# Kernel tuning notes

Measured on AMD Instinct MI355X. Metric: run time of the kernel, lower is better.

The kernel has to match this reference:

```python
import jax, jax.numpy as jnp
import numpy as np

# ---- fixed structural constants from the module source ----
BODY_PARTS = [[1, 2, 3], [4, 5, 6], [0, 7, 8, 9, 10], [11, 12, 13], [14, 15, 16]]
PART_EDGES = [[0, 2], [1, 2], [2, 3], [2, 4]]
N_JOINTS, N_PARTS = 17, 5
K_CHEB = 3  # ChebConv K=2 -> K+1 = 3 polynomial terms


def _pool_scatter_mats():
    # P[p, j] = 1/len(part_p) for j in part_p  (AdaptiveAvgPool1d(1) == mean)
    P = np.zeros((N_PARTS, N_JOINTS), np.float32)
    # S[j, p] = 1 if joint j belongs to part p (broadcast scatter)
    S = np.zeros((N_JOINTS, N_PARTS), np.float32)
    for p, idxs in enumerate(BODY_PARTS):
        for j in idxs:
            P[p, j] = 1.0 / len(idxs)
            S[j, p] = 1.0
    return jnp.asarray(P), jnp.asarray(S)


def _part_adj():
    # adj_mx_from_edges: symmetrize, add self loops, row-normalize
    A = np.zeros((N_PARTS, N_PARTS), np.float32)
    for i, j in PART_EDGES:
        A[i, j] = 1.0
    A = A + A.T  # edges are one-directional and disjoint -> symmetrize
    A = A + np.eye(N_PARTS, dtype=np.float32)
    A = A / A.sum(axis=1, keepdims=True)  # row-normalize
    return jnp.asarray(A)


def _cheb_basis(adj):
    # get_laplacian(normalize=True): L = I - D^{-1/2} A D^{-1/2}
    d_isqrt = jnp.sum(adj, axis=-1) ** (-0.5)
    L = jnp.eye(N_PARTS, dtype=adj.dtype) - (d_isqrt[:, None] * adj) * d_isqrt[None, :]
    I = jnp.eye(N_PARTS, dtype=adj.dtype)
    T2 = 2.0 * (L @ L) - I  # Chebyshev recurrence, K=2
    return jnp.stack([I, L, T2], axis=0)  # [3, 5, 5]


def setup_inputs() -> dict:
    key = jax.random.key(0)
    k1, k2 = jax.random.split(key)
    B, D = 8192, 512
    x = jax.random.normal(k1, (B, N_JOINTS, D), dtype=jnp.float32)
    # xavier-normal-like init for ChebConv weight [K+1, 1, in_c, out_c]
    scale = (2.0 / (D + D)) ** 0.5
    weight = jax.random.normal(k2, (K_CHEB, 1, D, D), dtype=jnp.float32) * scale
    bias = jnp.zeros((1, 1, D), dtype=jnp.float32)
    return {"x": x, "weight": weight, "bias": bias}


def reference(x, weight, bias):
    # x: [B, 17, D]; weight: [3, 1, D, D]; bias: [1, 1, D]
    P, S = _pool_scatter_mats()
    cheb = _cheb_basis(_part_adj())            # [3, 5, 5]
    part_feats = jnp.einsum('pj,bjd->bpd', P, x)              # part-wise mean pool
    prop = jnp.einsum('knm,bmd->kbnd', cheb, part_feats)      # Cheb propagation
    part_out = jnp.einsum('kbnd,kde->bne', prop, weight[:, 0]) + bias[0]  # [B, 5, D]
    return jnp.einsum('jp,bpd->bjd', S, part_out)             # broadcast to 17 joints
```

## Files before the change

kernel.cpp:

```cpp
#include <hip/hip_runtime.h>
#include <hip/hip_bf16.h>
#include <stdint.h>
#include <stddef.h>

typedef __attribute__((ext_vector_type(8))) short short8;
typedef __attribute__((ext_vector_type(4))) float f32x4;
typedef __attribute__((ext_vector_type(4))) unsigned int u32x4;

#define DIM   512
#define NJ    17
#define NPART 5
#define NB    8192
#define KDIM  1536
#define QROWS (NB*NPART)
#define ROWB  (KDIM*2)

struct Cheb { float c[3][5][5]; };

__device__ __forceinline__ void gload_lds16(const void* g, void* l) {
  __builtin_amdgcn_global_load_lds((__attribute__((address_space(1))) void*)(g),
                                   (__attribute__((address_space(3))) void*)(l),
                                   16, 0, 0);
}

__global__ __launch_bounds__(256) void pool_cheb_kernel(
    const float* __restrict__ x, __hip_bfloat16* __restrict__ Q, Cheb cb) {
  int gid = blockIdx.x * 256 + threadIdx.x;
  int b  = gid >> 7;
  int c4 = gid & 127;
  const float* xb = x + (size_t)b * (NJ * DIM) + (c4 << 2);

  f32x4 pf[5];
#pragma unroll
  for (int p = 0; p < 5; ++p) pf[p] = (f32x4){0.f, 0.f, 0.f, 0.f};

  constexpr int jpart[NJ] = {2,0,0,0,1,1,1,2,2,2,2,3,3,3,4,4,4};
#pragma unroll
  for (int j = 0; j < NJ; ++j) {
    f32x4 a = __builtin_nontemporal_load(
        reinterpret_cast<const f32x4*>(xb + j * DIM));
    pf[jpart[j]] += a;
  }
  constexpr float scl[5] = {1.f/3.f, 1.f/3.f, 0.2f, 1.f/3.f, 1.f/3.f};
#pragma unroll
  for (int p = 0; p < 5; ++p) pf[p] *= scl[p];

  char* qb = reinterpret_cast<char*>(Q);
  int cj = c4 >> 1;
#pragma unroll
  for (int k = 0; k < 3; ++k) {
#pragma unroll
    for (int n = 0; n < 5; ++n) {
      int row = b * 5 + n;
      f32x4 s = cb.c[k][n][0] * pf[0] + cb.c[k][n][1] * pf[1] +
                cb.c[k][n][2] * pf[2] + cb.c[k][n][3] * pf[3] +
                cb.c[k][n][4] * pf[4];
      alignas(8) __hip_bfloat16 o[4];
#pragma unroll
      for (int i = 0; i < 4; ++i) o[i] = __float2bfloat16(s[i]);
      int swc = (cj & 7) ^ (row & 7);
      size_t off = (size_t)row * ROWB + (size_t)(k * 8 + (cj >> 3)) * 128 +
                   (size_t)swc * 16 + (size_t)(c4 & 1) * 8;
      *reinterpret_cast<ushort4*>(qb + off) = *reinterpret_cast<const ushort4*>(o);
    }
  }
}

__global__ __launch_bounds__(256) void wt_kernel(
    const float* __restrict__ w, __hip_bfloat16* __restrict__ Wt) {
  int gid = blockIdx.x * 256 + threadIdx.x;
  int e = gid & 511;
  int chunk = gid >> 9;
  int kidx0 = chunk << 3;
  alignas(16) __hip_bfloat16 o[8];
#pragma unroll
  for (int i = 0; i < 8; ++i)
    o[i] = __float2bfloat16(w[(size_t)(kidx0 + i) * DIM + e]);
  int blk = kidx0 >> 6;
  int swc = ((kidx0 >> 3) & 7) ^ (e & 7);
  size_t off = (size_t)e * ROWB + (size_t)blk * 128 + (size_t)swc * 16;
  *reinterpret_cast<u32x4*>(reinterpret_cast<char*>(Wt) + off) =
      *reinterpret_cast<const u32x4*>(o);
}

__global__ __launch_bounds__(512, 2) void gemm_big_kernel(
    const __hip_bfloat16* __restrict__ Q, const __hip_bfloat16* __restrict__ Wt,
    const float* __restrict__ bias, float* __restrict__ out) {
  extern __shared__ __align__(16) char LDSbuf[];
  char* As0 = LDSbuf;
  char* As1 = LDSbuf + 40960;
  char* Bs0 = LDSbuf + 81920;
  char* Bs1 = LDSbuf + 114688;

  int tid  = threadIdx.x;
  int lane = tid & 63;
  int wave = tid >> 6;
  int wr = wave >> 1, wc = wave & 1;
  int m0 = blockIdx.y * 320;
  int n0 = blockIdx.x * 256;

  f32x4 acc[5][8] = {};

  const char* qb = reinterpret_cast<const char*>(Q);
  const char* wb = reinterpret_cast<const char*>(Wt);
  int sr8 = lane >> 3;
  int sc  = (lane & 7) * 16;

  const char* abase = qb + (size_t)(m0 + wave * 40 + sr8) * ROWB + sc;
  const char* bbase = wb + (size_t)(n0 + wave * 32 + sr8) * ROWB + sc;
  size_t aoff = wave * 5120;
  size_t boff = wave * 4096;

  auto stage = [&](char* Abuf, char* Bbuf, int ks) {
#pragma unroll
    for (int i = 0; i < 5; ++i)
      gload_lds16(abase + (size_t)i * (8 * ROWB) + (size_t)ks * 128,
                  Abuf + aoff + i * 1024);
#pragma unroll
    for (int i = 0; i < 4; ++i)
      gload_lds16(bbase + (size_t)i * (8 * ROWB) + (size_t)ks * 128,
                  Bbuf + boff + i * 1024);
  };

  auto compute = [&](const char* Abuf, const char* Bbuf) {
#pragma unroll
    for (int kk = 0; kk < 2; ++kk) {
      short8 af[5];
#pragma unroll
      for (int mi = 0; mi < 5; ++mi) {
        int r = wr * 80 + mi * 16 + (lane & 15);
        int c7 = (kk * 4 + (lane >> 4)) ^ (r & 7);
        af[mi] = *reinterpret_cast<const short8*>(Abuf + r * 128 + c7 * 16);
      }
#pragma unroll
      for (int h = 0; h < 2; ++h) {
        short8 bf[4];
#pragma unroll
        for (int nj = 0; nj < 4; ++nj) {
          int r = wc * 128 + (h * 4 + nj) * 16 + (lane & 15);
          int c7 = (kk * 4 + (lane >> 4)) ^ (r & 7);
          bf[nj] = *reinterpret_cast<const short8*>(Bbuf + r * 128 + c7 * 16);
        }
#pragma unroll
        for (int mi = 0; mi < 5; ++mi)
#pragma unroll
          for (int nj = 0; nj < 4; ++nj)
            acc[mi][h * 4 + nj] = __builtin_amdgcn_mfma_f32_16x16x32_bf16(
                af[mi], bf[nj], acc[mi][h * 4 + nj], 0, 0, 0);
      }
    }
  };

  stage(As0, Bs0, 0);
  __syncthreads();
  for (int ks = 0; ks < 22; ks += 2) {
    stage(As1, Bs1, ks + 1);
    compute(As0, Bs0);
    __syncthreads();
    stage(As0, Bs0, ks + 2);
    compute(As1, Bs1);
    __syncthreads();
  }
  stage(As1, Bs1, 23);
  compute(As0, Bs0);
  __syncthreads();
  compute(As1, Bs1);
  __syncthreads();

  float bs[8];
#pragma unroll
  for (int ni = 0; ni < 8; ++ni)
    bs[ni] = bias[n0 + wc * 128 + ni * 16 + (lane & 15)];

  char* eb = LDSbuf + wave * 8448;
  int halfsel = lane >> 5;
  int col4 = lane & 31;

#pragma unroll
  for (int mi = 0; mi < 5; ++mi) {
#pragma unroll
    for (int ni = 0; ni < 8; ++ni)
#pragma unroll
      for (int j = 0; j < 4; ++j) {
        int row = (lane >> 4) * 4 + j;
        *reinterpret_cast<float*>(
            eb + ((row * 132 + ni * 16 + (lane & 15)) << 2)) =
            acc[mi][ni][j] + bs[ni];
      }
#pragma unroll
    for (int rr = 0; rr < 8; ++rr) {
      int row = rr * 2 + halfsel;
      u32x4 v4 = *reinterpret_cast<const u32x4*>(
          eb + ((row * 132 + col4 * 4) << 2));
      int R = m0 + wr * 80 + mi * 16 + row;
      unsigned bb = (unsigned)R / 5u;
      int n = R - (int)bb * 5;
      unsigned mask = (n == 0) ? 0x0000Eu :
                      (n == 1) ? 0x00070u :
                      (n == 2) ? 0x00781u :
                      (n == 3) ? 0x03800u : 0x1C000u;
      float* op = out + (size_t)bb * (NJ * DIM) + (n0 + wc * 128 + col4 * 4);
      while (mask) {
        int jn = __builtin_ctz(mask);
        mask &= mask - 1;
        *reinterpret_cast<u32x4*>(op + jn * DIM) = v4;
      }
    }
  }
}

extern "C" void kernel_launch(void* const* d_in, const int* in_sizes, int n_in,
                              void* d_out, int out_size, void* d_ws, size_t ws_size,
                              hipStream_t stream) {
  const float* x    = (const float*)d_in[0];
  const float* w    = (const float*)d_in[1];
  const float* bias = (const float*)d_in[2];
  float* out = (float*)d_out;

  __hip_bfloat16* Q  = (__hip_bfloat16*)d_ws;
  __hip_bfloat16* Wt = (__hip_bfloat16*)((char*)d_ws + (size_t)QROWS * ROWB);

  Cheb cb;
  {
    double A[5][5] = {};
    const int e0[4] = {0, 1, 2, 2}, e1[4] = {2, 2, 3, 4};
    for (int t = 0; t < 4; ++t) { A[e0[t]][e1[t]] = 1.0; A[e1[t]][e0[t]] = 1.0; }
    for (int i = 0; i < 5; ++i) A[i][i] += 1.0;
    for (int i = 0; i < 5; ++i) {
      double rs = 0; for (int j = 0; j < 5; ++j) rs += A[i][j];
      for (int j = 0; j < 5; ++j) A[i][j] /= rs;
    }
    double L[5][5], T2[5][5];
    for (int i = 0; i < 5; ++i)
      for (int j = 0; j < 5; ++j) L[i][j] = (i == j ? 1.0 : 0.0) - A[i][j];
    for (int i = 0; i < 5; ++i)
      for (int j = 0; j < 5; ++j) {
        double s = 0; for (int m = 0; m < 5; ++m) s += L[i][m] * L[m][j];
        T2[i][j] = 2.0 * s - (i == j ? 1.0 : 0.0);
      }
    for (int i = 0; i < 5; ++i)
      for (int j = 0; j < 5; ++j) {
        cb.c[0][i][j] = (float)(i == j ? 1.0 : 0.0);
        cb.c[1][i][j] = (float)L[i][j];
        cb.c[2][i][j] = (float)T2[i][j];
      }
  }

  pool_cheb_kernel<<<(NB * 128) / 256, 256, 0, stream>>>(x, Q, cb);
  wt_kernel<<<(DIM * (KDIM / 8)) / 256, 256, 0, stream>>>(w, Wt);

  const int DYN_LDS = 147456;
  (void)hipFuncSetAttribute(
      reinterpret_cast<const void*>(gemm_big_kernel),
      hipFuncAttributeMaxDynamicSharedMemorySize, DYN_LDS);
  gemm_big_kernel<<<dim3(DIM / 256, QROWS / 320), 512, DYN_LDS, stream>>>(
      Q, Wt, bias, out);
}
```

Baseline: 170.6 us.

## Shrink GEMM block tile to 160x256 with 2x4 wave layout

Halves the GEMM block's M tile from 320 to 160 rows. The 8 waves are rearranged as 2x4 over M and N, so each wave now holds a 80x64 accumulator tile instead of 80x128. LDS per block drops from 144 KB to 104 KB and the grid doubles, which is meant to improve occupancy and load balance across CUs and cut register pressure. The cost is lower arithmetic intensity per block: more B-tile reloads from global memory and a smaller ratio of MFMA work to LDS reads.

```diff
diff --git a/kernel.cpp b/kernel.cpp
--- a/kernel.cpp
+++ b/kernel.cpp
@@ -88,44 +88,44 @@
     const float* __restrict__ bias, float* __restrict__ out) {
   extern __shared__ __align__(16) char LDSbuf[];
   char* As0 = LDSbuf;
-  char* As1 = LDSbuf + 40960;
-  char* Bs0 = LDSbuf + 81920;
-  char* Bs1 = LDSbuf + 114688;
+  char* As1 = LDSbuf + 20480;
+  char* Bs0 = LDSbuf + 40960;
+  char* Bs1 = LDSbuf + 73728;
 
   int tid  = threadIdx.x;
   int lane = tid & 63;
   int wave = tid >> 6;
-  int wr = wave >> 1, wc = wave & 1;
-  int m0 = blockIdx.y * 320;
+  int wr = wave >> 2, wc = wave & 3;
+  int m0 = blockIdx.y * 160;
   int n0 = blockIdx.x * 256;
 
-  f32x4 acc[5][8] = {};
+  f32x4 acc[5][4] = {};
 
   const char* qb = reinterpret_cast<const char*>(Q);
   const char* wb = reinterpret_cast<const char*>(Wt);
   int sr8 = lane >> 3;
   int sc  = (lane & 7) * 16;
 
-  const char* abase = qb + (size_t)(m0 + wave * 40 + sr8) * ROWB + sc;
-  const char* bbase = wb + (size_t)(n0 + wave * 32 + sr8) * ROWB + sc;
-  size_t aoff = wave * 5120;
-  size_t boff = wave * 4096;
-
   auto stage = [&](char* Abuf, char* Bbuf, int ks) {
 #pragma unroll
-    for (int i = 0; i < 5; ++i)
-      gload_lds16(abase + (size_t)i * (8 * ROWB) + (size_t)ks * 128,
-                  Abuf + aoff + i * 1024);
-#pragma unroll
-    for (int i = 0; i < 4; ++i)
-      gload_lds16(bbase + (size_t)i * (8 * ROWB) + (size_t)ks * 128,
-                  Bbuf + boff + i * 1024);
+    for (int i = 0; i < 3; ++i) {
+      int g = wave + i * 8;
+      if (g < 20)
+        gload_lds16(qb + (size_t)(m0 + g * 8 + sr8) * ROWB + (size_t)ks * 128 + sc,
+                    Abuf + g * 1024);
+    }
+#pragma unroll
+    for (int i = 0; i < 4; ++i) {
+      int g = wave + i * 8;
+      gload_lds16(wb + (size_t)(n0 + g * 8 + sr8) * ROWB + (size_t)ks * 128 + sc,
+                  Bbuf + g * 1024);
+    }
   };
 
   auto compute = [&](const char* Abuf, const char* Bbuf) {
 #pragma unroll
     for (int kk = 0; kk < 2; ++kk) {
-      short8 af[5];
+      short8 af[5], bf[4];
 #pragma unroll
       for (int mi = 0; mi < 5; ++mi) {
         int r = wr * 80 + mi * 16 + (lane & 15);
@@ -133,21 +133,17 @@
         af[mi] = *reinterpret_cast<const short8*>(Abuf + r * 128 + c7 * 16);
       }
 #pragma unroll
-      for (int h = 0; h < 2; ++h) {
-        short8 bf[4];
-#pragma unroll
-        for (int nj = 0; nj < 4; ++nj) {
-          int r = wc * 128 + (h * 4 + nj) * 16 + (lane & 15);
-          int c7 = (kk * 4 + (lane >> 4)) ^ (r & 7);
-          bf[nj] = *reinterpret_cast<const short8*>(Bbuf + r * 128 + c7 * 16);
-        }
-#pragma unroll
-        for (int mi = 0; mi < 5; ++mi)
-#pragma unroll
-          for (int nj = 0; nj < 4; ++nj)
-            acc[mi][h * 4 + nj] = __builtin_amdgcn_mfma_f32_16x16x32_bf16(
-                af[mi], bf[nj], acc[mi][h * 4 + nj], 0, 0, 0);
-      }
+      for (int nj = 0; nj < 4; ++nj) {
+        int r = wc * 64 + nj * 16 + (lane & 15);
+        int c7 = (kk * 4 + (lane >> 4)) ^ (r & 7);
+        bf[nj] = *reinterpret_cast<const short8*>(Bbuf + r * 128 + c7 * 16);
+      }
+#pragma unroll
+      for (int mi = 0; mi < 5; ++mi)
+#pragma unroll
+        for (int nj = 0; nj < 4; ++nj)
+          acc[mi][nj] = __builtin_amdgcn_mfma_f32_16x16x32_bf16(
+              af[mi], bf[nj], acc[mi][nj], 0, 0, 0);
     }
   };
 
@@ -167,39 +163,37 @@
   compute(As1, Bs1);
   __syncthreads();
 
-  float bs[8];
-#pragma unroll
-  for (int ni = 0; ni < 8; ++ni)
-    bs[ni] = bias[n0 + wc * 128 + ni * 16 + (lane & 15)];
-
-  char* eb = LDSbuf + wave * 8448;
-  int halfsel = lane >> 5;
-  int col4 = lane & 31;
+  float bs[4];
+#pragma unroll
+  for (int ni = 0; ni < 4; ++ni)
+    bs[ni] = bias[n0 + wc * 64 + ni * 16 + (lane & 15)];
+
+  char* eb = LDSbuf + wave * 4352;
+  int g4 = lane >> 4;
+  int cc = lane & 15;
 
 #pragma unroll
   for (int mi = 0; mi < 5; ++mi) {
 #pragma unroll
-    for (int ni = 0; ni < 8; ++ni)
-#pragma unroll
-      for (int j = 0; j < 4; ++j) {
-        int row = (lane >> 4) * 4 + j;
+    for (int ni = 0; ni < 4; ++ni)
+#pragma unroll
+      for (int j = 0; j < 4; ++j)
         *reinterpret_cast<float*>(
-            eb + ((row * 132 + ni * 16 + (lane & 15)) << 2)) =
+            eb + (((g4 * 4 + j) * 68 + ni * 16 + cc) << 2)) =
             acc[mi][ni][j] + bs[ni];
-      }
-#pragma unroll
-    for (int rr = 0; rr < 8; ++rr) {
-      int row = rr * 2 + halfsel;
+
+#pragma unroll
+    for (int t = 0; t < 4; ++t) {
       u32x4 v4 = *reinterpret_cast<const u32x4*>(
-          eb + ((row * 132 + col4 * 4) << 2));
-      int R = m0 + wr * 80 + mi * 16 + row;
+          eb + ((((t * 4 + g4) * 68) + cc * 4) << 2));
+      int R = m0 + wr * 80 + mi * 16 + t * 4 + g4;
       unsigned bb = (unsigned)R / 5u;
       int n = R - (int)bb * 5;
       unsigned mask = (n == 0) ? 0x0000Eu :
                       (n == 1) ? 0x00070u :
                       (n == 2) ? 0x00781u :
                       (n == 3) ? 0x03800u : 0x1C000u;
-      float* op = out + (size_t)bb * (NJ * DIM) + (n0 + wc * 128 + col4 * 4);
+      float* op = out + (size_t)bb * (NJ * DIM) + (n0 + wc * 64 + cc * 4);
       while (mask) {
         int jn = __builtin_ctz(mask);
         mask &= mask - 1;
@@ -249,10 +243,10 @@
   pool_cheb_kernel<<<(NB * 128) / 256, 256, 0, stream>>>(x, Q, cb);
   wt_kernel<<<(DIM * (KDIM / 8)) / 256, 256, 0, stream>>>(w, Wt);
 
-  const int DYN_LDS = 147456;
+  const int DYN_LDS = 106496;
   (void)hipFuncSetAttribute(
       reinterpret_cast<const void*>(gemm_big_kernel),
       hipFuncAttributeMaxDynamicSharedMemorySize, DYN_LDS);
-  gemm_big_kernel<<<dim3(DIM / 256, QROWS / 320), 512, DYN_LDS, stream>>>(
+  gemm_big_kernel<<<dim3(DIM / 256, QROWS / 160), 512, DYN_LDS, stream>>>(
       Q, Wt, bias, out);
 }
```

Measured after the change: 184.3 us. 8.0% more time.

## Load weight fragments directly from global in MFMA layout, shrink GEMM tile to 80x512

Applied to the files above, without the earlier changes.

The weight is now pre-packed into a fragment-ready layout, so the GEMM reads B operands straight from global memory (via L2) into registers instead of staging them through LDS. Each block covers all 512 output columns for 80 rows with 4 waves, and only the A tile is double-buffered in a small static LDS buffer. This cuts LDS traffic and footprint to allow more resident blocks, but every block re-reads the full 1.5 MB weight from cache, and B-load latency sits in the MFMA loop without prefetch.

```diff
diff --git a/kernel.cpp b/kernel.cpp
--- a/kernel.cpp
+++ b/kernel.cpp
@@ -66,113 +66,101 @@
   }
 }
 
-__global__ __launch_bounds__(256) void wt_kernel(
-    const float* __restrict__ w, __hip_bfloat16* __restrict__ Wt) {
-  int gid = blockIdx.x * 256 + threadIdx.x;
-  int e = gid & 511;
-  int chunk = gid >> 9;
-  int kidx0 = chunk << 3;
+__global__ __launch_bounds__(256) void wt3_kernel(
+    const float* __restrict__ w, __hip_bfloat16* __restrict__ Wt3) {
+  int c = blockIdx.x * 256 + threadIdx.x;
+  int e   = c & 511;
+  int kse = c >> 9;
+  int ks  = kse >> 3;
+  int kc  = kse & 7;
+  int k   = ks >> 3;
+  int d0  = (ks & 7) * 64 + kc * 8;
   alignas(16) __hip_bfloat16 o[8];
 #pragma unroll
   for (int i = 0; i < 8; ++i)
-    o[i] = __float2bfloat16(w[(size_t)(kidx0 + i) * DIM + e]);
-  int blk = kidx0 >> 6;
-  int swc = ((kidx0 >> 3) & 7) ^ (e & 7);
-  size_t off = (size_t)e * ROWB + (size_t)blk * 128 + (size_t)swc * 16;
-  *reinterpret_cast<u32x4*>(reinterpret_cast<char*>(Wt) + off) =
+    o[i] = __float2bfloat16(w[(size_t)k * (DIM * DIM) + (size_t)(d0 + i) * DIM + e]);
+  *reinterpret_cast<u32x4*>(reinterpret_cast<char*>(Wt3) + (size_t)c * 16) =
       *reinterpret_cast<const u32x4*>(o);
 }
 
-__global__ __launch_bounds__(512, 2) void gemm_big_kernel(
-    const __hip_bfloat16* __restrict__ Q, const __hip_bfloat16* __restrict__ Wt,
+__global__ __launch_bounds__(256, 2) void gemm_n512_kernel(
+    const __hip_bfloat16* __restrict__ Q, const __hip_bfloat16* __restrict__ Wt3,
     const float* __restrict__ bias, float* __restrict__ out) {
-  extern __shared__ __align__(16) char LDSbuf[];
-  char* As0 = LDSbuf;
-  char* As1 = LDSbuf + 40960;
-  char* Bs0 = LDSbuf + 81920;
-  char* Bs1 = LDSbuf + 114688;
+  __shared__ __align__(16) char LDS[33792];
+  char* As0 = LDS;
+  char* As1 = LDS + 10240;
 
   int tid  = threadIdx.x;
   int lane = tid & 63;
   int wave = tid >> 6;
-  int wr = wave >> 1, wc = wave & 1;
-  int m0 = blockIdx.y * 320;
-  int n0 = blockIdx.x * 256;
+  int wc   = wave;
+  int m0 = blockIdx.x * 80;
 
   f32x4 acc[5][8] = {};
 
   const char* qb = reinterpret_cast<const char*>(Q);
-  const char* wb = reinterpret_cast<const char*>(Wt);
+  const char* w3 = reinterpret_cast<const char*>(Wt3);
   int sr8 = lane >> 3;
   int sc  = (lane & 7) * 16;
 
-  const char* abase = qb + (size_t)(m0 + wave * 40 + sr8) * ROWB + sc;
-  const char* bbase = wb + (size_t)(n0 + wave * 32 + sr8) * ROWB + sc;
-  size_t aoff = wave * 5120;
-  size_t boff = wave * 4096;
-
-  auto stage = [&](char* Abuf, char* Bbuf, int ks) {
-#pragma unroll
-    for (int i = 0; i < 5; ++i)
-      gload_lds16(abase + (size_t)i * (8 * ROWB) + (size_t)ks * 128,
-                  Abuf + aoff + i * 1024);
-#pragma unroll
-    for (int i = 0; i < 4; ++i)
-      gload_lds16(bbase + (size_t)i * (8 * ROWB) + (size_t)ks * 128,
-                  Bbuf + boff + i * 1024);
+  auto stageA = [&](char* Abuf, int ks) {
+#pragma unroll
+    for (int i = 0; i < 3; ++i) {
+      int g = wave + i * 4;
+      if (g < 10)
+        gload_lds16(qb + (size_t)(m0 + g * 8 + sr8) * ROWB + (size_t)ks * 128 + sc,
+                    Abuf + g * 1024);
+    }
   };
 
-  auto compute = [&](const char* Abuf, const char* Bbuf) {
+  auto compute = [&](const char* Abuf, int ks) {
 #pragma unroll
     for (int kk = 0; kk < 2; ++kk) {
+      const char* bp = w3 + ((size_t)(ks * 8 + kk * 4 + (lane >> 4)) * 512 +
+                             (size_t)(wc * 128 + (lane & 15))) * 16;
+      short8 bf[8];
+#pragma unroll
+      for (int nj = 0; nj < 8; ++nj)
+        bf[nj] = *reinterpret_cast<const short8*>(bp + nj * 256);
+
       short8 af[5];
 #pragma unroll
       for (int mi = 0; mi < 5; ++mi) {
-        int r = wr * 80 + mi * 16 + (lane & 15);
+        int r = mi * 16 + (lane & 15);
         int c7 = (kk * 4 + (lane >> 4)) ^ (r & 7);
         af[mi] = *reinterpret_cast<const short8*>(Abuf + r * 128 + c7 * 16);
       }
 #pragma unroll
-      for (int h = 0; h < 2; ++h) {
-        short8 bf[4];
-#pragma unroll
-        for (int nj = 0; nj < 4; ++nj) {
-          int r = wc * 128 + (h * 4 + nj) * 16 + (lane & 15);
-          int c7 = (kk * 4 + (lane >> 4)) ^ (r & 7);
-          bf[nj] = *reinterpret_cast<const short8*>(Bbuf + r * 128 + c7 * 16);
-        }
-#pragma unroll
-        for (int mi = 0; mi < 5; ++mi)
-#pragma unroll
-          for (int nj = 0; nj < 4; ++nj)
-            acc[mi][h * 4 + nj] = __builtin_amdgcn_mfma_f32_16x16x32_bf16(
-                af[mi], bf[nj], acc[mi][h * 4 + nj], 0, 0, 0);
-      }
+      for (int mi = 0; mi < 5; ++mi)
+#pragma unroll
+        for (int nj = 0; nj < 8; ++nj)
+          acc[mi][nj] = __builtin_amdgcn_mfma_f32_16x16x32_bf16(
+              af[mi], bf[nj], acc[mi][nj], 0, 0, 0);
     }
   };
 
-  stage(As0, Bs0, 0);
+  stageA(As0, 0);
   __syncthreads();
   for (int ks = 0; ks < 22; ks += 2) {
-    stage(As1, Bs1, ks + 1);
-    compute(As0, Bs0);
+    stageA(As1, ks + 1);
+    compute(As0, ks);
     __syncthreads();
-    stage(As0, Bs0, ks + 2);
-    compute(As1, Bs1);
+    stageA(As0, ks + 2);
+    compute(As1, ks + 1);
     __syncthreads();
   }
-  stage(As1, Bs1, 23);
-  compute(As0, Bs0);
+  stageA(As1, 23);
+  compute(As0, 22);
   __syncthreads();
-  compute(As1, Bs1);
+  compute(As1, 23);
   __syncthreads();
 
   float bs[8];
 #pragma unroll
   for (int ni = 0; ni < 8; ++ni)
-    bs[ni] = bias[n0 + wc * 128 + ni * 16 + (lane & 15)];
-
-  char* eb = LDSbuf + wave * 8448;
+    bs[ni] = bias[wc * 128 + ni * 16 + (lane & 15)];
+
+  char* eb = LDS + wave * 8448;
   int halfsel = lane >> 5;
   int col4 = lane & 31;
 
@@ -192,14 +180,14 @@
       int row = rr * 2 + halfsel;
       u32x4 v4 = *reinterpret_cast<const u32x4*>(
           eb + ((row * 132 + col4 * 4) << 2));
-      int R = m0 + wr * 80 + mi * 16 + row;
+      int R = m0 + mi * 16 + row;
       unsigned bb = (unsigned)R / 5u;
       int n = R - (int)bb * 5;
       unsigned mask = (n == 0) ? 0x0000Eu :
                       (n == 1) ? 0x00070u :
                       (n == 2) ? 0x00781u :
                       (n == 3) ? 0x03800u : 0x1C000u;
-      float* op = out + (size_t)bb * (NJ * DIM) + (n0 + wc * 128 + col4 * 4);
+      float* op = out + (size_t)bb * (NJ * DIM) + (wc * 128 + col4 * 4);
       while (mask) {
         int jn = __builtin_ctz(mask);
         mask &= mask - 1;
@@ -217,8 +205,8 @@
   const float* bias = (const float*)d_in[2];
   float* out = (float*)d_out;
 
-  __hip_bfloat16* Q  = (__hip_bfloat16*)d_ws;
-  __hip_bfloat16* Wt = (__hip_bfloat16*)((char*)d_ws + (size_t)QROWS * ROWB);
+  __hip_bfloat16* Wt3 = (__hip_bfloat16*)d_ws;
+  __hip_bfloat16* Q   = (__hip_bfloat16*)((char*)d_ws + (2u << 20));
 
   Cheb cb;
   {
@@ -247,12 +235,6 @@
   }
 
   pool_cheb_kernel<<<(NB * 128) / 256, 256, 0, stream>>>(x, Q, cb);
-  wt_kernel<<<(DIM * (KDIM / 8)) / 256, 256, 0, stream>>>(w, Wt);
-
-  const int DYN_LDS = 147456;
-  (void)hipFuncSetAttribute(
-      reinterpret_cast<const void*>(gemm_big_kernel),
-      hipFuncAttributeMaxDynamicSharedMemorySize, DYN_LDS);
-  gemm_big_kernel<<<dim3(DIM / 256, QROWS / 320), 512, DYN_LDS, stream>>>(
-      Q, Wt, bias, out);
-}
+  wt3_kernel<<<384, 256, 0, stream>>>(w, Wt3);
+  gemm_n512_kernel<<<QROWS / 80, 256, 0, stream>>>(Q, Wt3, bias, out);
+}
```

Result: slower. 222.7 us (+30.5%).
